# Optimization experiments

Measured on AMD Instinct MI355X. Metric: run time of the kernel, lower is better.

Reference implementation:

```python
import jax, jax.numpy as jnp
import numpy as np

B, T, INPUT_DIM = 4, 2048, 256
D_MODEL = 512                       # hidden_dim // 2
EXPAND = 2
D_INNER = D_MODEL * EXPAND          # 1024
HEADDIM = 128                       # _pick_headdim(1024)
NHEADS = D_INNER // HEADDIM         # 8
DSTATE = 16
DCONV = 4
NLAYERS = 4
CONV_DIM = D_INNER + 2 * DSTATE            # 1056
D_IN_PROJ = 2 * D_INNER + 2 * DSTATE + NHEADS  # 2088
EPS = 1e-5


def _dir_params(key):
    ks = jax.random.split(key, 5)
    return dict(
        in_w=jax.random.normal(ks[0], (NLAYERS, D_IN_PROJ, D_MODEL)) * 0.02,
        conv_w=jax.random.normal(ks[1], (NLAYERS, CONV_DIM, DCONV)) * 0.1,
        conv_b=jnp.zeros((NLAYERS, CONV_DIM)),
        dt_bias=jnp.log(jnp.expm1(jax.random.uniform(ks[2], (NLAYERS, NHEADS), minval=1e-3, maxval=0.1))),
        A_log=jnp.log(jax.random.uniform(ks[3], (NLAYERS, NHEADS), minval=1.0, maxval=16.0)),
        D=jnp.ones((NLAYERS, NHEADS)),
        rms_w=jnp.ones((NLAYERS, D_INNER)),
        out_w=jax.random.normal(ks[4], (NLAYERS, D_MODEL, D_INNER)) * 0.02,
    )


def setup_inputs():
    key = jax.random.key(0)
    kx, ke, kf, kb = jax.random.split(key, 4)
    inp = {
        "x": jax.random.normal(kx, (B, T, INPUT_DIM), dtype=jnp.float32),
        "embed_w": jax.random.normal(ke, (D_MODEL, INPUT_DIM)) * 0.02,
        "embed_b": jnp.zeros((D_MODEL,)),
        "ln1_w": jnp.ones((D_MODEL,)), "ln1_b": jnp.zeros((D_MODEL,)),
        "lnout_w": jnp.ones((2 * D_MODEL,)), "lnout_b": jnp.zeros((2 * D_MODEL,)),
    }
    for tag, p in (("f", _dir_params(kf)), ("b", _dir_params(kb))):
        for k, v in p.items():
            inp[f"{k}_{tag}"] = v
    return inp


def _silu(x):
    return x * jax.nn.sigmoid(x)


def _layernorm(x, w, b):
    m = jnp.mean(x, -1, keepdims=True)
    v = jnp.mean((x - m) ** 2, -1, keepdims=True)
    return (x - m) * jax.lax.rsqrt(v + EPS) * w + b


def _mamba2(h, in_w, conv_w, conv_b, dt_bias, A_log, Dh, rms_w, out_w):
    """One Mamba2 (SSD) block: in_proj -> causal depthwise conv -> selective scan
    -> gated RMSNorm -> out_proj. Sequential scan is math-equivalent to the
    chunked SSD kernel."""
    Bb, Tt, _ = h.shape
    zxbcdt = jnp.einsum('btd,ed->bte', h, in_w)
    z = zxbcdt[..., :D_INNER]
    xBC = zxbcdt[..., D_INNER:D_INNER + CONV_DIM]
    dt = zxbcdt[..., D_INNER + CONV_DIM:]                      # [B,T,H]
    # causal depthwise conv over time (kernel DCONV), then silu
    xc = jax.lax.conv_general_dilated(
        jnp.transpose(xBC, (0, 2, 1)), conv_w[:, None, :], (1,),
        [(DCONV - 1, 0)], feature_group_count=CONV_DIM)
    xBC = _silu(jnp.transpose(xc, (0, 2, 1)) + conv_b)
    xs = xBC[..., :D_INNER].reshape(Bb, Tt, NHEADS, HEADDIM)   # [B,T,H,P]
    Bm = xBC[..., D_INNER:D_INNER + DSTATE]                    # [B,T,N]
    Cm = xBC[..., D_INNER + DSTATE:]                           # [B,T,N]
    dt = jax.nn.softplus(dt + dt_bias)                         # [B,T,H]
    dA = jnp.exp(dt * (-jnp.exp(A_log)))                       # [B,T,H]
    xdt = xs * dt[..., None]                                   # [B,T,H,P]
    tm = lambda a: jnp.moveaxis(a, 1, 0)                       # time-major

    def step(s, inp):
        dA_t, xdt_t, B_t, C_t = inp
        s = dA_t[:, :, None, None] * s + xdt_t[..., None] * B_t[:, None, None, :]
        return s, jnp.einsum('bhpn,bn->bhp', s, C_t)

    s0 = jnp.zeros((Bb, NHEADS, HEADDIM, DSTATE), h.dtype)
    _, ys = jax.lax.scan(step, s0, (tm(dA), tm(xdt), tm(Bm), tm(Cm)))
    y = jnp.moveaxis(ys, 0, 1) + Dh[None, None, :, None] * xs
    y = y.reshape(Bb, Tt, D_INNER)
    g = y * _silu(z)                                           # gated RMSNorm (norm after gate)
    g = g * jax.lax.rsqrt(jnp.mean(g * g, -1, keepdims=True) + EPS) * rms_w
    return jnp.einsum('bti,oi->bto', g, out_w)


def _forward(x, embed_w, embed_b, ln1_w, ln1_b, lnout_w, lnout_b,
             in_w_f, conv_w_f, conv_b_f, dt_bias_f, A_log_f, D_f, rms_w_f, out_w_f,
             in_w_b, conv_w_b, conv_b_b, dt_bias_b, A_log_b, D_b, rms_w_b, out_w_b):
    h = _layernorm(jnp.einsum('bti,oi->bto', x, embed_w) + embed_b, ln1_w, ln1_b)
    h_f, h_b = h, h[:, ::-1]
    for i in range(NLAYERS):
        h_f = _mamba2(h_f, in_w_f[i], conv_w_f[i], conv_b_f[i], dt_bias_f[i],
                      A_log_f[i], D_f[i], rms_w_f[i], out_w_f[i]) + h_f
    for i in range(NLAYERS):
        h_b = _mamba2(h_b, in_w_b[i], conv_w_b[i], conv_b_b[i], dt_bias_b[i],
                      A_log_b[i], D_b[i], rms_w_b[i], out_w_b[i]) + h_b
    out = jnp.concatenate([h_f, h_b[:, ::-1]], axis=-1)        # [B,T,2*D_MODEL]
    return _layernorm(out, lnout_w, lnout_b)


def reference(x, embed_w, embed_b, ln1_w, ln1_b, lnout_w, lnout_b,
              in_w_f, conv_w_f, conv_b_f, dt_bias_f, A_log_f, D_f, rms_w_f, out_w_f,
              in_w_b, conv_w_b, conv_b_b, dt_bias_b, A_log_b, D_b, rms_w_b, out_w_b):
    return _forward(x, embed_w, embed_b, ln1_w, ln1_b, lnout_w, lnout_b,
                    in_w_f, conv_w_f, conv_b_f, dt_bias_f, A_log_f, D_f, rms_w_f, out_w_f,
                    in_w_b, conv_w_b, conv_b_b, dt_bias_b, A_log_b, D_b, rms_w_b, out_w_b)
```

## Files before the change

### kernel.cpp

```cpp
#include <hip/hip_runtime.h>
#include <hip/hip_bf16.h>
#include <math.h>

#define BB 4
#define TT 2048
#define BT 8192
#define DM 512
#define DI 1024
#define NH 8
#define HD 128
#define DS 16
#define CONVD 1056
#define DPROJ 2088
#define NL 4
#define CL 128
#define NCH 16
#define NE 131072

typedef __hip_bfloat16 bf16;
typedef __attribute__((ext_vector_type(8))) short short8;
typedef __attribute__((ext_vector_type(4))) float f32x4;

static __device__ __forceinline__ float b2f_raw(short v){
  union { unsigned u; float f; } c; c.u = ((unsigned)(unsigned short)v) << 16; return c.f;
}

static __device__ __forceinline__ void red2(float& a, float& b, float* sb){
  #pragma unroll
  for (int o = 32; o; o >>= 1){ a += __shfl_down(a, o); b += __shfl_down(b, o); }
  int w = threadIdx.x >> 6;
  if ((threadIdx.x & 63) == 0){ sb[w] = a; sb[4+w] = b; }
  __syncthreads();
  a = sb[0]+sb[1]+sb[2]+sb[3];
  b = sb[4]+sb[5]+sb[6]+sb[7];
}

__global__ __launch_bounds__(256) void detect_dtype(const void* x, int* flagp){
  __shared__ int cnt;
  if (threadIdx.x == 0) cnt = 0;
  __syncthreads();
  const bf16* p = (const bf16*)x;
  int bad = 0;
  for (int i = threadIdx.x; i < 32768; i += 256){
    float v = __bfloat162float(p[i]);
    if (!isfinite(v) || fabsf(v) > 1e4f) bad++;
  }
  atomicAdd(&cnt, bad);
  __syncthreads();
  if (threadIdx.x == 0) *flagp = (cnt > 100) ? 1 : 0;
}

__global__ __launch_bounds__(256) void convert_in(const void* src, bf16* dst, int n,
                                                  const int* flagp){
  int f = *flagp;
  for (int i = blockIdx.x*256 + threadIdx.x; i < n; i += gridDim.x*256){
    if (f) dst[i] = __float2bfloat16(((const float*)src)[i]);
    else   dst[i] = ((const bf16*)src)[i];
  }
}

template<int OP>
__global__ __launch_bounds__(256) void gemm_nt(
    const bf16* __restrict__ A, const bf16* __restrict__ W0, const bf16* __restrict__ W1,
    bf16* C, const bf16* X, float* aux,
    int M, int N, int K, int lda, long sA, long sC)
{
  const int z = blockIdx.z;
  const bf16* Az = A + (long)z * sA;
  const bf16* W = z ? W1 : W0;
  const int m0 = blockIdx.x * 128, n0 = blockIdx.y * 128;
  __shared__ __align__(16) bf16 As[128*32];
  __shared__ __align__(16) bf16 Bs[128*32];
  const int tid  = threadIdx.x;
  const int lane = tid & 63, wv = tid >> 6;
  const int wm = wv >> 1, wn = wv & 1;
  const int quad = lane >> 4, l16 = lane & 15;
  const int strow = tid >> 2;
  const int stbyt = (tid & 3) * 16;

  f32x4 acc[4][4];
  #pragma unroll
  for (int i=0;i<4;i++)
    #pragma unroll
    for (int j=0;j<4;j++) acc[i][j] = (f32x4){0.f,0.f,0.f,0.f};

  for (int k0 = 0; k0 < K; k0 += 32){
    short8 va[2], vb[2];
    #pragma unroll
    for (int is = 0; is < 2; ++is){
      int r = is*64 + strow;
      va[is] = *(const short8*)((const char*)(Az + (long)(m0 + r)*lda + k0) + stbyt);
      int rn = n0 + r; rn = rn < N ? rn : N-1;
      vb[is] = *(const short8*)((const char*)(W + (long)rn*K + k0) + stbyt);
    }
    __syncthreads();
    #pragma unroll
    for (int is = 0; is < 2; ++is){
      int r = is*64 + strow;
      *(short8*)((char*)As + (long)r*64 + stbyt) = va[is];
      *(short8*)((char*)Bs + (long)r*64 + stbyt) = vb[is];
    }
    __syncthreads();
    short8 af[4], bfr[4];
    #pragma unroll
    for (int mi=0;mi<4;mi++) af[mi]  = *(const short8*)((const char*)As + (long)(wm*64+mi*16+l16)*64 + quad*16);
    #pragma unroll
    for (int ni=0;ni<4;ni++) bfr[ni] = *(const short8*)((const char*)Bs + (long)(wn*64+ni*16+l16)*64 + quad*16);
    #pragma unroll
    for (int mi=0;mi<4;mi++)
      #pragma unroll
      for (int ni=0;ni<4;ni++)
        acc[mi][ni] = __builtin_amdgcn_mfma_f32_16x16x32_bf16(af[mi], bfr[ni], acc[mi][ni], 0, 0, 0);
  }

  bf16* Cz = C + (long)z * sC;
  const bf16* Xz = (OP==2) ? (X + (long)z * sC) : X;
  #pragma unroll
  for (int mi=0;mi<4;mi++){
    #pragma unroll
    for (int ni=0;ni<4;ni++){
      #pragma unroll
      for (int r=0;r<4;r++){
        int row = m0 + wm*64 + mi*16 + quad*4 + r;
        int col = n0 + wn*64 + ni*16 + l16;
        if (col < N){
          float v = acc[mi][ni][r];
          if (OP==1) v += __bfloat162float(X[col]);
          if (OP==2) v += __bfloat162float(Xz[(long)row*N + col]);
          Cz[(long)row*N + col] = __float2bfloat16(v);
          if (OP==3 && col >= DPROJ-8)
            aux[(long)z*BT*8 + (long)row*8 + (col-(DPROJ-8))] = v;
        }
      }
    }
  }
}

__global__ __launch_bounds__(256) void embed_ln(const bf16* __restrict__ hp,
    const bf16* __restrict__ w, const bf16* __restrict__ bb, bf16* __restrict__ h)
{
  __shared__ float sb[8];
  int bt = blockIdx.x; int b = bt >> 11, t = bt & 2047;
  const bf16* r = hp + (long)bt*DM;
  int c0 = threadIdx.x, c1 = threadIdx.x + 256;
  float v0 = __bfloat162float(r[c0]);
  float v1 = __bfloat162float(r[c1]);
  float s = v0+v1, ss = v0*v0+v1*v1;
  red2(s, ss, sb);
  float m = s / DM;
  float var = ss / DM - m*m;
  float rs = rsqrtf(fmaxf(var, 0.f) + 1e-5f);
  float a0 = (v0-m)*rs*__bfloat162float(w[c0]) + __bfloat162float(bb[c0]);
  float a1 = (v1-m)*rs*__bfloat162float(w[c1]) + __bfloat162float(bb[c1]);
  bf16* o0 = h + (long)bt*DM;
  bf16* o1 = h + ((long)BT + (long)b*TT + (TT-1-t)) * DM;
  o0[c0] = __float2bfloat16(a0); o0[c1] = __float2bfloat16(a1);
  o1[c0] = __float2bfloat16(a0); o1[c1] = __float2bfloat16(a1);
}

__global__ __launch_bounds__(256) void conv_silu(const bf16* __restrict__ zx,
    const bf16* __restrict__ cw0, const bf16* __restrict__ cw1,
    const bf16* __restrict__ cb0, const bf16* __restrict__ cb1,
    bf16* __restrict__ xbc)
{
  int bt = blockIdx.x, dir = blockIdx.y;
  int t = bt & 2047;
  const bf16* cw = dir ? cw1 : cw0;
  const bf16* cb = dir ? cb1 : cb0;
  const bf16* zr = zx + ((long)dir*BT + bt)*DPROJ + DI;
  bf16* orow = xbc + ((long)dir*BT + bt)*CONVD;
  for (int c = threadIdx.x; c < CONVD; c += 256){
    float acc = __bfloat162float(cb[c]);
    #pragma unroll
    for (int j=0;j<4;j++){
      int ts = t - 3 + j;
      if (ts >= 0)
        acc += __bfloat162float(cw[c*4+j]) * __bfloat162float(zr[(long)(j-3)*DPROJ + c]);
    }
    float sg = 1.f / (1.f + expf(-acc));
    orow[c] = __float2bfloat16(acc * sg);
  }
}

__global__ __launch_bounds__(256) void dt_kernel(const float* __restrict__ draw,
    const bf16* __restrict__ db0, const bf16* __restrict__ db1,
    const bf16* __restrict__ al0, const bf16* __restrict__ al1,
    float2* __restrict__ dadt)
{
  int idx = blockIdx.x*256 + threadIdx.x;
  int dir = idx >> 16, r = idx & 65535;
  int bt = r >> 3, h = r & 7;
  int b = bt >> 11, t = bt & 2047;
  float x = draw[idx] + __bfloat162float((dir?db1:db0)[h]);
  float sp = (x > 20.f) ? x : log1pf(expf(x));
  float a = expf(-expf(__bfloat162float((dir?al1:al0)[h])) * sp);
  long o = (((long)dir*BB + b)*NH + h)*TT + t;
  float2 v; v.x = a; v.y = sp;
  dadt[o] = v;
}

#define SC_LOAD(X,BV,CV,DD,T0) do{ \
  _Pragma("unroll") \
  for (int _i=0;_i<4;_i++){ \
    const bf16* _rr = xr + (long)((T0)+_i)*CONVD; \
    X[_i]  = __bfloat162float(_rr[h*HD + p]); \
    BV[_i] = *(const short8*)(_rr + DI + half*8); \
    CV[_i] = *(const short8*)(_rr + DI + DS + half*8); \
    DD[_i] = ddr[(T0)+_i]; \
  } }while(0)

#define SC_STEP(X,BV,CV,DD,T0) do{ \
  _Pragma("unroll") \
  for (int _i=0;_i<4;_i++){ \
    float _dav = DD[_i].x, _dtv = DD[_i].y; \
    float _xdt = X[_i] * _dtv; \
    float _acc = 0.f; \
    _Pragma("unroll") \
    for (int _n=0;_n<8;_n++){ \
      s[_n] = fmaf(_dav, s[_n], _xdt * b2f_raw(BV[_i][_n])); \
      _acc  = fmaf(s[_n], b2f_raw(CV[_i][_n]), _acc); } \
    _acc += __shfl_xor(_acc, 1); \
    if (!half) xw[(long)((T0)+_i)*CONVD + h*HD + p] = __float2bfloat16(_acc + Dv*X[_i]); \
  } }while(0)

#define CH_LOAD(X,BV,DD,T0) do{ \
  _Pragma("unroll") \
  for (int _i=0;_i<4;_i++){ \
    const bf16* _rr = xr + (long)((T0)+_i)*CONVD; \
    X[_i]  = __bfloat162float(_rr[h*HD + p]); \
    BV[_i] = *(const short8*)(_rr + DI + half*8); \
    DD[_i] = ddr[(T0)+_i]; \
  } }while(0)

#define CH_STEP(X,BV,DD) do{ \
  _Pragma("unroll") \
  for (int _i=0;_i<4;_i++){ \
    float _dav = DD[_i].x, _dtv = DD[_i].y; \
    float _xdt = X[_i] * _dtv; \
    _Pragma("unroll") \
    for (int _n=0;_n<8;_n++) \
      s[_n] = fmaf(_dav, s[_n], _xdt * b2f_raw(BV[_i][_n])); \
    pacc *= _dav; \
  } }while(0)

__global__ __launch_bounds__(256) void chunk_local(const bf16* __restrict__ xbc,
    const float2* __restrict__ dadt, float* __restrict__ SC, float* __restrict__ Pc)
{
  int c = blockIdx.x, dbh = blockIdx.y;
  int dir = dbh >> 5, b = (dbh >> 3) & 3, h = dbh & 7;
  int tid = threadIdx.x, p = tid >> 1, half = tid & 1;
  const bf16* xr = xbc + ((long)dir*BT + (long)b*TT) * CONVD;
  const float2* ddr = dadt + (((long)dir*BB + b)*NH + h)*TT;
  float s[8];
  #pragma unroll
  for (int n=0;n<8;n++) s[n] = 0.f;
  float pacc = 1.f;
  const int c0 = c*CL;

  float xA[4], xB2[4];
  short8 BA[4], BB2[4];
  float2 dA_[4], dB_[4];

  CH_LOAD(xA,BA,dA_, c0);
  for (int t0 = c0; t0 < c0+CL; t0 += 8){
    CH_LOAD(xB2,BB2,dB_, t0+4);
    CH_STEP(xA,BA,dA_);
    if (t0+8 < c0+CL) CH_LOAD(xA,BA,dA_, t0+8);
    CH_STEP(xB2,BB2,dB_);
  }
  long e = (long)dbh*2048 + p*16 + half*8;
  #pragma unroll
  for (int n=0;n<8;n++) SC[(long)c*NE + e + n] = s[n];
  if (tid == 0) Pc[dbh*NCH + c] = pacc;
}

__global__ __launch_bounds__(256) void chunk_combine(float* __restrict__ SC,
    const float* __restrict__ Pc)
{
  int e = blockIdx.x*256 + threadIdx.x;
  int dbh = e >> 11;
  float s = 0.f;
  #pragma unroll
  for (int c=0;c<NCH;c++){
    float tmp = SC[(long)c*NE + e];
    SC[(long)c*NE + e] = s;
    s = Pc[dbh*NCH + c]*s + tmp;
  }
}

__global__ __launch_bounds__(256) void chunk_apply(bf16* __restrict__ xbc,
    const float2* __restrict__ dadt, const float* __restrict__ SC,
    const bf16* __restrict__ D0, const bf16* __restrict__ D1)
{
  int c = blockIdx.x, dbh = blockIdx.y;
  int dir = dbh >> 5, b = (dbh >> 3) & 3, h = dbh & 7;
  int tid = threadIdx.x, p = tid >> 1, half = tid & 1;
  const bf16* xr = xbc + ((long)dir*BT + (long)b*TT) * CONVD;
  bf16* xw = xbc + ((long)dir*BT + (long)b*TT) * CONVD;
  const float2* ddr = dadt + (((long)dir*BB + b)*NH + h)*TT;
  float Dv = __bfloat162float(dir ? D1[h] : D0[h]);
  long e = (long)dbh*2048 + p*16 + half*8;
  float s[8];
  #pragma unroll
  for (int n=0;n<8;n++) s[n] = SC[(long)c*NE + e + n];
  const int c0 = c*CL;

  float xA[4], xB2[4];
  short8 BA[4], BB2[4], CA[4], CB2[4];
  float2 dA_[4], dB_[4];

  SC_LOAD(xA,BA,CA,dA_, c0);
  for (int t0 = c0; t0 < c0+CL; t0 += 8){
    SC_LOAD(xB2,BB2,CB2,dB_, t0+4);
    SC_STEP(xA,BA,CA,dA_, t0);
    if (t0+8 < c0+CL) SC_LOAD(xA,BA,CA,dA_, t0+8);
    SC_STEP(xB2,BB2,CB2,dB_, t0+4);
  }
}

__global__ __launch_bounds__(256) void gate_rms(const bf16* __restrict__ xbc, bf16* zx,
    const bf16* __restrict__ rw0, const bf16* __restrict__ rw1)
{
  __shared__ float sb[8];
  int bt = blockIdx.x, dir = blockIdx.y;
  const bf16* yr = xbc + ((long)dir*BT + bt)*CONVD;
  bf16* zr = zx + ((long)dir*BT + bt)*DPROJ;
  const bf16* rw = dir ? rw1 : rw0;
  float gv[4], ss = 0.f, dummy = 0.f;
  #pragma unroll
  for (int i=0;i<4;i++){
    int c = threadIdx.x + i*256;
    float yv = __bfloat162float(yr[c]);
    float zv = __bfloat162float(zr[c]);
    float sg = 1.f/(1.f+expf(-zv));
    gv[i] = yv * zv * sg;
    ss += gv[i]*gv[i];
  }
  red2(ss, dummy, sb);
  float sc = rsqrtf(ss / DI + 1e-5f);
  #pragma unroll
  for (int i=0;i<4;i++){
    int c = threadIdx.x + i*256;
    zr[c] = __float2bfloat16(gv[i]*sc*__bfloat162float(rw[c]));
  }
}

__global__ __launch_bounds__(256) void final_ln(const bf16* __restrict__ h,
    const bf16* __restrict__ lw, const bf16* __restrict__ lb, void* out,
    int mode, const int* flagp)
{
  __shared__ float sb[8];
  int bt = blockIdx.x; int b = bt >> 11, t = bt & 2047;
  int f32out = mode ? *flagp : 0;
  const bf16* rf = h + (long)bt*DM;
  const bf16* rb = h + ((long)BT + (long)b*TT + (TT-1-t))*DM;
  float v[4], s = 0.f, ss = 0.f;
  #pragma unroll
  for (int i=0;i<4;i++){
    int c = threadIdx.x + i*256;
    v[i] = __bfloat162float(c < DM ? rf[c] : rb[c-DM]);
    s += v[i]; ss += v[i]*v[i];
  }
  red2(s, ss, sb);
  float m = s / (2*DM);
  float var = ss / (2*DM) - m*m;
  float rs = rsqrtf(fmaxf(var, 0.f) + 1e-5f);
  #pragma unroll
  for (int i=0;i<4;i++){
    int c = threadIdx.x + i*256;
    float o = (v[i]-m)*rs*__bfloat162float(lw[c]) + __bfloat162float(lb[c]);
    if (f32out) ((float*)out)[(long)bt*(2*DM) + c] = o;
    else        ((bf16*)out)[(long)bt*(2*DM) + c] = __float2bfloat16(o);
  }
}

extern "C" void kernel_launch(void* const* d_in, const int* in_sizes, int n_in,
                              void* d_out, int out_size, void* d_ws, size_t ws_size,
                              hipStream_t stream)
{
  char* wsp = (char*)d_ws;
  auto take = [&](size_t bytes){ char* p = wsp; wsp += (bytes + 63) & ~(size_t)63; return p; };
  int*   flagp = (int*)  take(4);
  bf16*  h     = (bf16*) take((size_t)2*BT*DM*2);
  bf16*  zx    = (bf16*) take((size_t)2*BT*DPROJ*2);
  bf16*  xbc   = (bf16*) take((size_t)2*BT*CONVD*2);
  float2* dadt = (float2*)take((size_t)2*BB*NH*TT*8);
  float* draw  = (float*)take((size_t)2*BT*NH*4);
  float* Pc    = (float*)take((size_t)64*NCH*4);
  float* SC    = (float*)take((size_t)NCH*NE*4);
  size_t needDirect = (size_t)(wsp - (char*)d_ws);

  static const int cnt[23] = {
    BT*256, DM*256, DM, DM, DM, 2*DM, 2*DM,
    NL*DPROJ*DM, NL*CONVD*4, NL*CONVD, NL*NH, NL*NH, NL*NH, NL*DI, NL*DM*DI,
    NL*DPROJ*DM, NL*CONVD*4, NL*CONVD, NL*NH, NL*NH, NL*NH, NL*DI, NL*DM*DI };
  bf16* canon[23];
  for (int i = 0; i < 23; ++i) canon[i] = (bf16*)take((size_t)cnt[i]*2);
  size_t needFull = (size_t)(wsp - (char*)d_ws);

  const int convMode = (ws_size >= needFull) ? 1 : 0;

  const bf16* in[23];
  if (convMode){
    detect_dtype<<<1,256,0,stream>>>(d_in[0], flagp);
    for (int i = 0; i < 23; ++i){
      int grid = (cnt[i] + 255)/256; if (grid > 2048) grid = 2048;
      convert_in<<<grid,256,0,stream>>>(d_in[i], canon[i], cnt[i], flagp);
      in[i] = canon[i];
    }
  } else {
    for (int i = 0; i < 23; ++i) in[i] = (const bf16*)d_in[i];
  }

  const bf16* x       = in[0];
  const bf16* embed_w = in[1];
  const bf16* embed_b = in[2];
  const bf16* ln1_w   = in[3];
  const bf16* ln1_b   = in[4];
  const bf16* lnout_w = in[5];
  const bf16* lnout_b = in[6];
  const bf16* in_w[2]   = {in[7],  in[15]};
  const bf16* conv_w[2] = {in[8],  in[16]};
  const bf16* conv_b[2] = {in[9],  in[17]};
  const bf16* dt_b[2]   = {in[10], in[18]};
  const bf16* A_log[2]  = {in[11], in[19]};
  const bf16* Dp[2]     = {in[12], in[20]};
  const bf16* rms_w[2]  = {in[13], in[21]};
  const bf16* out_w[2]  = {in[14], in[22]};

  bf16* hpre = xbc;

  gemm_nt<1><<<dim3(64,4,1),256,0,stream>>>(x, embed_w, embed_w, hpre, embed_b, nullptr,
                                            BT, DM, 256, 256, 0, 0);
  embed_ln<<<dim3(BT),256,0,stream>>>(hpre, ln1_w, ln1_b, h);

  for (int i = 0; i < NL; ++i){
    gemm_nt<3><<<dim3(64,17,2),256,0,stream>>>(h, in_w[0]+(size_t)i*DPROJ*DM, in_w[1]+(size_t)i*DPROJ*DM,
        zx, nullptr, draw, BT, DPROJ, DM, DM, (long)BT*DM, (long)BT*DPROJ);
    conv_silu<<<dim3(BT,2),256,0,stream>>>(zx, conv_w[0]+(size_t)i*CONVD*4, conv_w[1]+(size_t)i*CONVD*4,
        conv_b[0]+(size_t)i*CONVD, conv_b[1]+(size_t)i*CONVD, xbc);
    dt_kernel<<<dim3(512),256,0,stream>>>(draw, dt_b[0]+i*NH, dt_b[1]+i*NH,
        A_log[0]+i*NH, A_log[1]+i*NH, dadt);
    chunk_local<<<dim3(NCH,64),256,0,stream>>>(xbc, dadt, SC, Pc);
    chunk_combine<<<dim3(NE/256),256,0,stream>>>(SC, Pc);
    chunk_apply<<<dim3(NCH,64),256,0,stream>>>(xbc, dadt, SC, Dp[0]+i*NH, Dp[1]+i*NH);
    gate_rms<<<dim3(BT,2),256,0,stream>>>(xbc, zx, rms_w[0]+(size_t)i*DI, rms_w[1]+(size_t)i*DI);
    gemm_nt<2><<<dim3(64,4,2),256,0,stream>>>(zx, out_w[0]+(size_t)i*DM*DI, out_w[1]+(size_t)i*DM*DI,
        h, h, nullptr, BT, DM, DI, DPROJ, (long)BT*DPROJ, (long)BT*DM);
  }

  final_ln<<<dim3(BT),256,0,stream>>>(h, lnout_w, lnout_b, d_out, convMode, flagp);
  (void)needDirect; (void)in_sizes; (void)n_in; (void)out_size;
}
```

Baseline: 1.367 ms.

## Use direct global-to-LDS loads in GEMM and vectorize conv and gate kernels

The GEMM tile loads now use global_load_lds to write global data straight into shared memory, skipping the staging through registers. The conv_silu and gate_rms kernels are rewritten so each thread handles four channels with vector loads and stores. The aim is fewer load instructions and fewer register round-trips. The direct-to-LDS path puts the barrier at the start of each k step and removes the overlap of register prefetch with the previous tile's compute, which could expose global latency.

```diff
diff --git a/kernel.cpp b/kernel.cpp
--- a/kernel.cpp
+++ b/kernel.cpp
@@ -19,7 +19,11 @@
 
 typedef __hip_bfloat16 bf16;
 typedef __attribute__((ext_vector_type(8))) short short8;
+typedef __attribute__((ext_vector_type(4))) short short4v;
 typedef __attribute__((ext_vector_type(4))) float f32x4;
+
+#define AS_G __attribute__((address_space(1)))
+#define AS_L __attribute__((address_space(3)))
 
 static __device__ __forceinline__ float b2f_raw(short v){
   union { unsigned u; float f; } c; c.u = ((unsigned)(unsigned short)v) << 16; return c.f;
@@ -75,8 +79,8 @@
   const int lane = tid & 63, wv = tid >> 6;
   const int wm = wv >> 1, wn = wv & 1;
   const int quad = lane >> 4, l16 = lane & 15;
-  const int strow = tid >> 2;
-  const int stbyt = (tid & 3) * 16;
+  const int srow = lane >> 2;
+  const int skb  = (lane & 3) * 16;
 
   f32x4 acc[4][4];
   #pragma unroll
@@ -85,20 +89,17 @@
     for (int j=0;j<4;j++) acc[i][j] = (f32x4){0.f,0.f,0.f,0.f};
 
   for (int k0 = 0; k0 < K; k0 += 32){
-    short8 va[2], vb[2];
+    __syncthreads();
     #pragma unroll
     for (int is = 0; is < 2; ++is){
-      int r = is*64 + strow;
-      va[is] = *(const short8*)((const char*)(Az + (long)(m0 + r)*lda + k0) + stbyt);
+      int r = is*64 + wv*16 + srow;
+      const char* gA = (const char*)(Az + (long)(m0 + r)*lda + k0) + skb;
+      char* lA = (char*)As + (long)(is*64 + wv*16)*64;
+      __builtin_amdgcn_global_load_lds((const AS_G void*)gA, (AS_L void*)lA, 16, 0, 0);
       int rn = n0 + r; rn = rn < N ? rn : N-1;
-      vb[is] = *(const short8*)((const char*)(W + (long)rn*K + k0) + stbyt);
-    }
-    __syncthreads();
-    #pragma unroll
-    for (int is = 0; is < 2; ++is){
-      int r = is*64 + strow;
-      *(short8*)((char*)As + (long)r*64 + stbyt) = va[is];
-      *(short8*)((char*)Bs + (long)r*64 + stbyt) = vb[is];
+      const char* gB = (const char*)(W + (long)rn*K + k0) + skb;
+      char* lB = (char*)Bs + (long)(is*64 + wv*16)*64;
+      __builtin_amdgcn_global_load_lds((const AS_G void*)gB, (AS_L void*)lB, 16, 0, 0);
     }
     __syncthreads();
     short8 af[4], bfr[4];
@@ -169,16 +170,31 @@
   const bf16* cb = dir ? cb1 : cb0;
   const bf16* zr = zx + ((long)dir*BT + bt)*DPROJ + DI;
   bf16* orow = xbc + ((long)dir*BT + bt)*CONVD;
-  for (int c = threadIdx.x; c < CONVD; c += 256){
-    float acc = __bfloat162float(cb[c]);
+  for (int cg = threadIdx.x; cg < CONVD/4; cg += 256){
+    int c = cg*4;
+    short8 w01 = *(const short8*)(cw + c*4);
+    short8 w23 = *(const short8*)(cw + c*4 + 8);
+    short4v bi = *(const short4v*)(cb + c);
+    float acc[4];
+    #pragma unroll
+    for (int k=0;k<4;k++) acc[k] = b2f_raw(bi[k]);
     #pragma unroll
     for (int j=0;j<4;j++){
-      int ts = t - 3 + j;
-      if (ts >= 0)
-        acc += __bfloat162float(cw[c*4+j]) * __bfloat162float(zr[(long)(j-3)*DPROJ + c]);
+      if (t - 3 + j >= 0){
+        short4v xv = *(const short4v*)(zr + (long)(j-3)*DPROJ + c);
+        acc[0] = fmaf(b2f_raw(w01[j]),   b2f_raw(xv[0]), acc[0]);
+        acc[1] = fmaf(b2f_raw(w01[4+j]), b2f_raw(xv[1]), acc[1]);
+        acc[2] = fmaf(b2f_raw(w23[j]),   b2f_raw(xv[2]), acc[2]);
+        acc[3] = fmaf(b2f_raw(w23[4+j]), b2f_raw(xv[3]), acc[3]);
+      }
     }
-    float sg = 1.f / (1.f + expf(-acc));
-    orow[c] = __float2bfloat16(acc * sg);
+    short4v ov;
+    #pragma unroll
+    for (int k=0;k<4;k++){
+      float sg = 1.f / (1.f + expf(-acc[k]));
+      ov[k] = (short)__bfloat16_as_ushort(__float2bfloat16(acc[k] * sg));
+    }
+    *(short4v*)(orow + c) = ov;
   }
 }
 
@@ -326,23 +342,26 @@
   const bf16* yr = xbc + ((long)dir*BT + bt)*CONVD;
   bf16* zr = zx + ((long)dir*BT + bt)*DPROJ;
   const bf16* rw = dir ? rw1 : rw0;
+  int c = threadIdx.x*4;
+  short4v yv4 = *(const short4v*)(yr + c);
+  short4v zv4 = *(const short4v*)(zr + c);
+  short4v rw4 = *(const short4v*)(rw + c);
   float gv[4], ss = 0.f, dummy = 0.f;
   #pragma unroll
-  for (int i=0;i<4;i++){
-    int c = threadIdx.x + i*256;
-    float yv = __bfloat162float(yr[c]);
-    float zv = __bfloat162float(zr[c]);
+  for (int k=0;k<4;k++){
+    float yv = b2f_raw(yv4[k]);
+    float zv = b2f_raw(zv4[k]);
     float sg = 1.f/(1.f+expf(-zv));
-    gv[i] = yv * zv * sg;
-    ss += gv[i]*gv[i];
+    gv[k] = yv * zv * sg;
+    ss += gv[k]*gv[k];
   }
   red2(ss, dummy, sb);
   float sc = rsqrtf(ss / DI + 1e-5f);
-  #pragma unroll
-  for (int i=0;i<4;i++){
-    int c = threadIdx.x + i*256;
-    zr[c] = __float2bfloat16(gv[i]*sc*__bfloat162float(rw[c]));
-  }
+  short4v ov;
+  #pragma unroll
+  for (int k=0;k<4;k++)
+    ov[k] = (short)__bfloat16_as_ushort(__float2bfloat16(gv[k]*sc*b2f_raw(rw4[k])));
+  *(short4v*)(zr + c) = ov;
 }
 
 __global__ __launch_bounds__(256) void final_ln(const bf16* __restrict__ h,
```

Result: faster. 1.237 ms (-9.5%).
